# Kernel optimization log

Hardware: AMD Instinct MI355X
Metric: run time of the kernel (lower is better)

## Reference

```python
import jax, jax.numpy as jnp
import numpy as np

WS = (8, 8)
NUM_HEADS = 6
DIM = 192
HEAD_DIM = DIM // NUM_HEADS
SCALE = HEAD_DIM ** -0.5


def _relative_position_index(ws):
    ch, cw = np.arange(ws[0]), np.arange(ws[1])
    coords = np.stack(np.meshgrid(ch, cw, indexing='ij'))          # (2, Wh, Ww)
    cf = coords.reshape(2, -1)                                      # (2, N)
    rel = cf[:, :, None] - cf[:, None, :]                           # (2, N, N)
    rel = rel.transpose(1, 2, 0).copy()                             # (N, N, 2)
    rel[:, :, 0] += ws[0] - 1
    rel[:, :, 1] += ws[1] - 1
    rel[:, :, 0] *= 2 * ws[1] - 1
    return rel.sum(-1)                                              # (N, N)

REL_IDX = jnp.asarray(_relative_position_index(WS))


def setup_inputs() -> dict:
    key = jax.random.key(0)
    ks = jax.random.split(key, 9)
    B_, N, C = 8192, WS[0] * WS[1], DIM
    x1 = jax.random.normal(ks[0], (B_, N, C), jnp.float32)
    x2 = jax.random.normal(ks[1], (B_, N, C), jnp.float32)
    mask = jnp.zeros((1024, N, N), jnp.float32)
    q_w = jax.random.normal(ks[2], (C, C), jnp.float32) * 0.02
    q_b = jnp.zeros((C,), jnp.float32)
    kv_w = jax.random.normal(ks[3], (2 * C, C), jnp.float32) * 0.02
    kv_b = jnp.zeros((2 * C,), jnp.float32)
    proj_w = jax.random.normal(ks[4], (C, C), jnp.float32) * 0.02
    proj_b = jnp.zeros((C,), jnp.float32)
    table = jax.random.normal(ks[5], ((2 * WS[0] - 1) * (2 * WS[1] - 1), NUM_HEADS), jnp.float32) * 0.02
    return dict(x1=x1, x2=x2, mask=mask, q_w=q_w, q_b=q_b, kv_w=kv_w,
                kv_b=kv_b, proj_w=proj_w, proj_b=proj_b, table=table)


def reference(x1, x2, mask, q_w, q_b, kv_w, kv_b, proj_w, proj_b, table):
    B_, N, C = x1.shape
    H, hd = NUM_HEADS, HEAD_DIM
    q = (x1 @ q_w.T + q_b).reshape(B_, N, H, hd).transpose(0, 2, 1, 3)   # (B_,H,N,hd)
    kv = (x2 @ kv_w.T + kv_b).reshape(B_, N, 2, H, hd).transpose(2, 0, 3, 1, 4)
    k, v = kv[0], kv[1]                                                   # (B_,H,N,hd)
    attn = jnp.einsum('bhnd,bhmd->bhnm', q * SCALE, k)                    # (B_,H,N,N)
    bias = table[REL_IDX.reshape(-1)].reshape(N, N, H).transpose(2, 0, 1)  # (H,N,N)
    attn = attn + bias[None]
    nW = mask.shape[0]
    attn = attn.reshape(B_ // nW, nW, H, N, N) + mask[None, :, None]
    attn = jax.nn.softmax(attn.reshape(B_, H, N, N), axis=-1)
    out = jnp.einsum('bhnm,bhmd->bhnd', attn, v).transpose(0, 2, 1, 3).reshape(B_, N, C)
    return out @ proj_w.T + proj_b
```

## Files before the change

### kernel.cpp

```cpp
#include <hip/hip_runtime.h>

typedef __bf16 bf16_t;
typedef __bf16 bf16x8 __attribute__((ext_vector_type(8)));
typedef __bf16 bf16x4 __attribute__((ext_vector_type(4)));
typedef __bf16 bf16x2 __attribute__((ext_vector_type(2)));
typedef float f32x4 __attribute__((ext_vector_type(4)));

#define SCALE 0.17677669529663687f

__device__ __forceinline__ f32x4 mfma16(bf16x8 a, bf16x8 b, f32x4 c) {
  return __builtin_amdgcn_mfma_f32_16x16x32_bf16(a, b, c, 0, 0, 0);
}

__device__ __forceinline__ int swz(int row, int colByte, int strideB) {
  return row * strideB + ((((colByte >> 4) ^ (row & 7)) << 4) | (colByte & 15));
}

__device__ __forceinline__ void barrier_nd() {
  asm volatile("s_waitcnt lgkmcnt(0)" ::: "memory");
  __builtin_amdgcn_s_barrier();
  asm volatile("" ::: "memory");
}

union CvtU { bf16x2 h; unsigned int u; };
union PaU { unsigned int u[4]; bf16x8 v; };

__global__ void prep(const float* __restrict__ qw, const float* __restrict__ kvw,
                     const float* __restrict__ pw, bf16_t* __restrict__ wsb) {
  int i = blockIdx.x * 256 + threadIdx.x;
#pragma unroll
  for (int j = 0; j < 4; ++j) {
    int e = i * 4 + j;
    float v;
    if (e < 36864) v = qw[e] * SCALE;
    else if (e < 110592) v = kvw[e - 36864];
    else v = pw[e - 110592];
    wsb[e] = (bf16_t)v;
  }
}

template <bool WS>
__device__ __forceinline__ bf16x8 ldw(const bf16_t* __restrict__ wb,
                                      const float* __restrict__ wf, int off) {
  if constexpr (WS) {
    return *(const bf16x8*)(wb + off);
  } else {
    const float4* p = (const float4*)(wf + off);
    float4 a = p[0], c = p[1];
    bf16x8 r;
    r[0] = (bf16_t)a.x; r[1] = (bf16_t)a.y; r[2] = (bf16_t)a.z; r[3] = (bf16_t)a.w;
    r[4] = (bf16_t)c.x; r[5] = (bf16_t)c.y; r[6] = (bf16_t)c.z; r[7] = (bf16_t)c.w;
    return r;
  }
}

template <bool WS>
__global__ __launch_bounds__(512, 2) void wca_main(
    const float* __restrict__ x1, const float* __restrict__ x2,
    const float* __restrict__ mask,
    const float* __restrict__ qw_f, const float* __restrict__ qb,
    const float* __restrict__ kvw_f, const float* __restrict__ kvb,
    const float* __restrict__ pw_f, const float* __restrict__ pb,
    const float* __restrict__ table,
    const bf16_t* __restrict__ wsb,
    float* __restrict__ out) {
  extern __shared__ char smem[];
  char* RA = smem;
  char* RK = smem + 49152;
  char* RV = smem + 98304;

  const int t = threadIdx.x;
  const int w = t >> 6, l = t & 63, lo = l & 15, hi = l >> 4;
  const int win0 = 2 * blockIdx.x;

  const bf16_t* q_wb = wsb;
  const bf16_t* kv_wb = wsb + 36864;
  const bf16_t* p_wb = wsb + 110592;

  {
    const float4* s2a = (const float4*)(x2 + (size_t)win0 * 12288);
    const float4* s2b = (const float4*)(x2 + (size_t)(win0 + 1) * 12288);
    float4 ld[12];
#pragma unroll
    for (int it = 0; it < 3; ++it) {
      int idx = it * 512 + t;
      ld[4 * it + 0] = s2a[2 * idx]; ld[4 * it + 1] = s2a[2 * idx + 1];
      ld[4 * it + 2] = s2b[2 * idx]; ld[4 * it + 3] = s2b[2 * idx + 1];
    }
#pragma unroll
    for (int it = 0; it < 3; ++it) {
      int idx = it * 512 + t;
      int n = idx / 24, g = idx - n * 24;
      bf16x8 v;
      float4 a = ld[4 * it + 0], c = ld[4 * it + 1];
      v[0] = (bf16_t)a.x; v[1] = (bf16_t)a.y; v[2] = (bf16_t)a.z; v[3] = (bf16_t)a.w;
      v[4] = (bf16_t)c.x; v[5] = (bf16_t)c.y; v[6] = (bf16_t)c.z; v[7] = (bf16_t)c.w;
      *(bf16x8*)(RA + swz(n, g * 16, 384)) = v;
      a = ld[4 * it + 2]; c = ld[4 * it + 3];
      v[0] = (bf16_t)a.x; v[1] = (bf16_t)a.y; v[2] = (bf16_t)a.z; v[3] = (bf16_t)a.w;
      v[4] = (bf16_t)c.x; v[5] = (bf16_t)c.y; v[6] = (bf16_t)c.z; v[7] = (bf16_t)c.w;
      *(bf16x8*)(RA + swz(64 + n, g * 16, 384)) = v;
    }
  }
  barrier_nd();

  {
    bf16x8 wA[6][3];
#pragma unroll
    for (int kk = 0; kk < 6; ++kk)
#pragma unroll
      for (int ct = 0; ct < 3; ++ct) {
        int row = w * 48 + ct * 16 + lo;
        wA[kk][ct] = ldw<WS>(kv_wb, kvw_f, row * 192 + kk * 32 + hi * 8);
      }
    for (int wv = 0; wv < 2; ++wv) {
      f32x4 acc[4][3];
#pragma unroll
      for (int rt = 0; rt < 4; ++rt)
#pragma unroll
        for (int ct = 0; ct < 3; ++ct) { f32x4 z = {0.f, 0.f, 0.f, 0.f}; acc[rt][ct] = z; }
#pragma unroll
      for (int kk = 0; kk < 6; ++kk) {
        bf16x8 a[4];
#pragma unroll
        for (int rt = 0; rt < 4; ++rt)
          a[rt] = *(const bf16x8*)(RA + swz(wv * 64 + rt * 16 + lo, (kk * 4 + hi) * 16, 384));
#pragma unroll
        for (int rt = 0; rt < 4; ++rt)
#pragma unroll
          for (int ct = 0; ct < 3; ++ct)
            acc[rt][ct] = mfma16(a[rt], wA[kk][ct], acc[rt][ct]);
      }
      if (w < 4) {
#pragma unroll
        for (int ct = 0; ct < 3; ++ct) {
          int och = w * 48 + ct * 16 + lo;
          float bv = kvb[och];
#pragma unroll
          for (int rt = 0; rt < 4; ++rt)
#pragma unroll
            for (int i = 0; i < 4; ++i)
              *(bf16_t*)(RK + swz(wv * 64 + rt * 16 + hi * 4 + i, och * 2, 384)) =
                  (bf16_t)(acc[rt][ct][i] + bv);
        }
      } else {
#pragma unroll
        for (int ct = 0; ct < 3; ++ct) {
          int och = (w - 4) * 48 + ct * 16 + lo;
          float bv = kvb[192 + och];
#pragma unroll
          for (int rt = 0; rt < 4; ++rt) {
            int n0 = rt * 16 + hi * 4;
            bf16x4 pk;
#pragma unroll
            for (int i = 0; i < 4; ++i) pk[i] = (bf16_t)(acc[rt][ct][i] + bv);
            *(bf16x4*)(RV + wv * 24576 + swz(och, n0 * 2, 128)) = pk;
          }
        }
      }
    }
  }
  barrier_nd();

  {
    const int wv = w >> 2, rt2 = (w >> 1) & 1, cg = w & 1;
    const float* x1w = x1 + (size_t)(win0 + wv) * 12288;
    f32x4 acc[2][6];
#pragma unroll
    for (int rt = 0; rt < 2; ++rt)
#pragma unroll
      for (int ct = 0; ct < 6; ++ct) { f32x4 z = {0.f, 0.f, 0.f, 0.f}; acc[rt][ct] = z; }
#pragma unroll
    for (int kh = 0; kh < 2; ++kh) {
      float4 xf[2][3][2];
#pragma unroll
      for (int rt = 0; rt < 2; ++rt) {
        const float4* p = (const float4*)(x1w + (rt2 * 32 + rt * 16 + lo) * 192);
#pragma unroll
        for (int k2 = 0; k2 < 3; ++k2) {
          xf[rt][k2][0] = p[(kh * 3 + k2) * 8 + hi * 2];
          xf[rt][k2][1] = p[(kh * 3 + k2) * 8 + hi * 2 + 1];
        }
      }
      bf16x8 wB[3][6];
#pragma unroll
      for (int k2 = 0; k2 < 3; ++k2)
#pragma unroll
        for (int ct = 0; ct < 6; ++ct) {
          int col = cg * 96 + ct * 16 + lo;
          wB[k2][ct] = ldw<WS>(q_wb, qw_f, col * 192 + (kh * 3 + k2) * 32 + hi * 8);
        }
#pragma unroll
      for (int k2 = 0; k2 < 3; ++k2)
#pragma unroll
        for (int rt = 0; rt < 2; ++rt) {
          bf16x8 a;
          float4 xa = xf[rt][k2][0], xb = xf[rt][k2][1];
          a[0] = (bf16_t)xa.x; a[1] = (bf16_t)xa.y; a[2] = (bf16_t)xa.z; a[3] = (bf16_t)xa.w;
          a[4] = (bf16_t)xb.x; a[5] = (bf16_t)xb.y; a[6] = (bf16_t)xb.z; a[7] = (bf16_t)xb.w;
#pragma unroll
          for (int ct = 0; ct < 6; ++ct) acc[rt][ct] = mfma16(a, wB[k2][ct], acc[rt][ct]);
        }
    }
#pragma unroll
    for (int ct = 0; ct < 6; ++ct) {
      int col = cg * 96 + ct * 16 + lo;
      float qbs = qb[col] * SCALE;
#pragma unroll
      for (int rt = 0; rt < 2; ++rt)
#pragma unroll
        for (int i = 0; i < 4; ++i) {
          int row = wv * 64 + rt2 * 32 + rt * 16 + hi * 4 + i;
          float val = WS ? (acc[rt][ct][i] + qbs) : (acc[rt][ct][i] + qb[col]) * SCALE;
          *(bf16_t*)(RA + swz(row, col * 2, 384)) = (bf16_t)val;
        }
    }
  }
  barrier_nd();

  {
    const int wv = w >> 2, rt32 = (w >> 1) & 1, hh = w & 1;
    const int win = win0 + wv;
    const float* maskb = mask + (size_t)(win & 1023) * 4096;
    f32x4 mk[2][4];
    int ridx[2][4][4];
#pragma unroll
    for (int rts = 0; rts < 2; ++rts) {
      int r = rt32 * 32 + rts * 16 + lo;
#pragma unroll
      for (int ct = 0; ct < 4; ++ct) {
        mk[rts][ct] = *(const f32x4*)(maskb + r * 64 + ct * 16 + hi * 4);
#pragma unroll
        for (int i = 0; i < 4; ++i) {
          int c = ct * 16 + hi * 4 + i;
          ridx[rts][ct][i] = (((r >> 3) - (c >> 3) + 7) * 15 + ((r & 7) - (c & 7) + 7)) * 6;
        }
      }
    }
#pragma unroll
    for (int hq = 0; hq < 3; ++hq) {
      const int h = hh * 3 + hq;
#pragma unroll
      for (int rts = 0; rts < 2; ++rts) {
        const int rbase = rt32 * 32 + rts * 16;
        const int r = rbase + lo;
        bf16x8 qa = *(const bf16x8*)(RA + swz(wv * 64 + r, h * 64 + hi * 16, 384));
        f32x4 s[4];
#pragma unroll
        for (int ct = 0; ct < 4; ++ct) {
          f32x4 ci;
#pragma unroll
          for (int i = 0; i < 4; ++i) ci[i] = table[ridx[rts][ct][i] + h];
          ci += mk[rts][ct];
          bf16x8 ka = *(const bf16x8*)(RK + swz(wv * 64 + ct * 16 + lo, h * 64 + hi * 16, 384));
          s[ct] = mfma16(ka, qa, ci);
        }
        float mx = -1e30f;
#pragma unroll
        for (int ct = 0; ct < 4; ++ct)
#pragma unroll
          for (int i = 0; i < 4; ++i) mx = fmaxf(mx, s[ct][i]);
        mx = fmaxf(mx, __shfl_xor(mx, 16));
        mx = fmaxf(mx, __shfl_xor(mx, 32));
        float sum = 0.f;
#pragma unroll
        for (int ct = 0; ct < 4; ++ct)
#pragma unroll
          for (int i = 0; i < 4; ++i) {
            float p = __expf(s[ct][i] - mx);
            s[ct][i] = p;
            sum += p;
          }
        sum += __shfl_xor(sum, 16);
        sum += __shfl_xor(sum, 32);
        float rinv = 1.0f / sum;
        unsigned int word[4][2];
#pragma unroll
        for (int ct = 0; ct < 4; ++ct)
#pragma unroll
          for (int i2 = 0; i2 < 2; ++i2) {
            CvtU cu;
            cu.h[0] = (bf16_t)(s[ct][2 * i2] * rinv);
            cu.h[1] = (bf16_t)(s[ct][2 * i2 + 1] * rinv);
            word[ct][i2] = cu.u;
          }
        f32x4 o0 = {0.f, 0.f, 0.f, 0.f}, o1 = {0.f, 0.f, 0.f, 0.f};
#pragma unroll
        for (int k2 = 0; k2 < 2; ++k2) {
          PaU pa;
#pragma unroll
          for (int j2 = 0; j2 < 4; ++j2) {
            int src = lo + ((hi & 1) << 5) + ((j2 >> 1) << 4);
            unsigned int wa = (unsigned int)__shfl((int)word[2 * k2][j2 & 1], src);
            unsigned int wb = (unsigned int)__shfl((int)word[2 * k2 + 1][j2 & 1], src);
            pa.u[j2] = (hi & 2) ? wb : wa;
          }
          bf16x8 v0 = *(const bf16x8*)(RV + wv * 24576 + swz(h * 32 + lo, k2 * 64 + hi * 16, 128));
          bf16x8 v1 = *(const bf16x8*)(RV + wv * 24576 + swz(h * 32 + 16 + lo, k2 * 64 + hi * 16, 128));
          o0 = mfma16(pa.v, v0, o0);
          o1 = mfma16(pa.v, v1, o1);
        }
#pragma unroll
        for (int i = 0; i < 4; ++i) {
          int rr = wv * 64 + rbase + hi * 4 + i;
          *(bf16_t*)(RA + swz(rr, h * 64 + lo * 2, 384)) = (bf16_t)o0[i];
          *(bf16_t*)(RA + swz(rr, h * 64 + 32 + lo * 2, 384)) = (bf16_t)o1[i];
        }
      }
    }
  }
  barrier_nd();

  {
    const int wv = w >> 2, cgo = w & 3;
    bf16x8 wO[6][3];
#pragma unroll
    for (int kk = 0; kk < 6; ++kk)
#pragma unroll
      for (int ct = 0; ct < 3; ++ct) {
        int col = cgo * 48 + ct * 16 + lo;
        wO[kk][ct] = ldw<WS>(p_wb, pw_f, col * 192 + kk * 32 + hi * 8);
      }
    f32x4 acc[4][3];
#pragma unroll
    for (int rt = 0; rt < 4; ++rt)
#pragma unroll
      for (int ct = 0; ct < 3; ++ct) { f32x4 z = {0.f, 0.f, 0.f, 0.f}; acc[rt][ct] = z; }
#pragma unroll
    for (int kk = 0; kk < 6; ++kk) {
      bf16x8 a[4];
#pragma unroll
      for (int rt = 0; rt < 4; ++rt)
        a[rt] = *(const bf16x8*)(RA + swz(wv * 64 + rt * 16 + lo, (kk * 4 + hi) * 16, 384));
#pragma unroll
      for (int rt = 0; rt < 4; ++rt)
#pragma unroll
        for (int ct = 0; ct < 3; ++ct)
          acc[rt][ct] = mfma16(a[rt], wO[kk][ct], acc[rt][ct]);
    }
    float* outp = out + (size_t)(win0 + wv) * 12288;
#pragma unroll
    for (int ct = 0; ct < 3; ++ct) {
      int col = cgo * 48 + ct * 16 + lo;
      float bv = pb[col];
#pragma unroll
      for (int rt = 0; rt < 4; ++rt)
#pragma unroll
        for (int i = 0; i < 4; ++i)
          outp[(rt * 16 + hi * 4 + i) * 192 + col] = acc[rt][ct][i] + bv;
    }
  }
}

extern "C" void kernel_launch(void* const* d_in, const int* in_sizes, int n_in,
                              void* d_out, int out_size, void* d_ws, size_t ws_size,
                              hipStream_t stream) {
  const float* x1 = (const float*)d_in[0];
  const float* x2 = (const float*)d_in[1];
  const float* mask = (const float*)d_in[2];
  const float* qw = (const float*)d_in[3];
  const float* qb = (const float*)d_in[4];
  const float* kvw = (const float*)d_in[5];
  const float* kvb = (const float*)d_in[6];
  const float* pw = (const float*)d_in[7];
  const float* pb = (const float*)d_in[8];
  const float* table = (const float*)d_in[9];
  float* out = (float*)d_out;
  bf16_t* wsb = (bf16_t*)d_ws;
  const int LDS_BYTES = 147456;
  if (ws_size >= 294912) {
    prep<<<144, 256, 0, stream>>>(qw, kvw, pw, wsb);
    wca_main<true><<<4096, 512, LDS_BYTES, stream>>>(x1, x2, mask, qw, qb, kvw, kvb,
                                                     pw, pb, table, wsb, out);
  } else {
    wca_main<false><<<4096, 512, LDS_BYTES, stream>>>(x1, x2, mask, qw, qb, kvw, kvb,
                                                      pw, pb, table, wsb, out);
  }
}
```

Baseline: 651.9 us.

## Make kernel persistent over windows with async global-to-LDS prefetch of inputs

Replaces the one-block-per-two-windows launch (4096 blocks) with 256 persistent blocks that each loop over 32 windows, one window per iteration. The x2 and x1 fp32 tiles are fetched into an LDS staging buffer with global_load_lds DMA, so the next window's loads overlap the current window's compute. This is meant to hide global memory latency and cut per-block launch and setup overhead. In exchange each block handles a single window at a time, LDS use drops, there are more barriers per window, and 256 blocks may under-fill the GPU's compute units and leave occupancy low.

```diff
diff --git a/kernel.cpp b/kernel.cpp
--- a/kernel.cpp
+++ b/kernel.cpp
@@ -1,4 +1,5 @@
 #include <hip/hip_runtime.h>
+#include <stdint.h>
 
 typedef __bf16 bf16_t;
 typedef __bf16 bf16x8 __attribute__((ext_vector_type(8)));
@@ -20,6 +21,18 @@
   asm volatile("s_waitcnt lgkmcnt(0)" ::: "memory");
   __builtin_amdgcn_s_barrier();
   asm volatile("" ::: "memory");
+}
+__device__ __forceinline__ void barrier_vm() {
+  asm volatile("s_waitcnt vmcnt(0) lgkmcnt(0)" ::: "memory");
+  __builtin_amdgcn_s_barrier();
+  asm volatile("" ::: "memory");
+}
+
+__device__ __forceinline__ void dma16(const float* g, char* lds) {
+  __builtin_amdgcn_global_load_lds(
+      (const __attribute__((address_space(1))) uint32_t*)(uintptr_t)g,
+      (__attribute__((address_space(3))) uint32_t*)(uint32_t)(uintptr_t)lds,
+      16, 0, 0);
 }
 
 union CvtU { bf16x2 h; unsigned int u; };
@@ -66,54 +79,64 @@
     float* __restrict__ out) {
   extern __shared__ char smem[];
   char* RA = smem;
-  char* RK = smem + 49152;
-  char* RV = smem + 98304;
+  char* RK = smem + 24576;
+  char* RV = smem + 49152;
+  char* PF = smem + 73728;
 
   const int t = threadIdx.x;
   const int w = t >> 6, l = t & 63, lo = l & 15, hi = l >> 4;
-  const int win0 = 2 * blockIdx.x;
+  const int bid = blockIdx.x;
+  const int rtB = w & 3, cgB = w >> 2;
 
   const bf16_t* q_wb = wsb;
   const bf16_t* kv_wb = wsb + 36864;
   const bf16_t* p_wb = wsb + 110592;
 
   {
-    const float4* s2a = (const float4*)(x2 + (size_t)win0 * 12288);
-    const float4* s2b = (const float4*)(x2 + (size_t)(win0 + 1) * 12288);
-    float4 ld[12];
-#pragma unroll
-    for (int it = 0; it < 3; ++it) {
-      int idx = it * 512 + t;
-      ld[4 * it + 0] = s2a[2 * idx]; ld[4 * it + 1] = s2a[2 * idx + 1];
-      ld[4 * it + 2] = s2b[2 * idx]; ld[4 * it + 3] = s2b[2 * idx + 1];
-    }
-#pragma unroll
-    for (int it = 0; it < 3; ++it) {
-      int idx = it * 512 + t;
-      int n = idx / 24, g = idx - n * 24;
-      bf16x8 v;
-      float4 a = ld[4 * it + 0], c = ld[4 * it + 1];
-      v[0] = (bf16_t)a.x; v[1] = (bf16_t)a.y; v[2] = (bf16_t)a.z; v[3] = (bf16_t)a.w;
-      v[4] = (bf16_t)c.x; v[5] = (bf16_t)c.y; v[6] = (bf16_t)c.z; v[7] = (bf16_t)c.w;
-      *(bf16x8*)(RA + swz(n, g * 16, 384)) = v;
-      a = ld[4 * it + 2]; c = ld[4 * it + 3];
-      v[0] = (bf16_t)a.x; v[1] = (bf16_t)a.y; v[2] = (bf16_t)a.z; v[3] = (bf16_t)a.w;
-      v[4] = (bf16_t)c.x; v[5] = (bf16_t)c.y; v[6] = (bf16_t)c.z; v[7] = (bf16_t)c.w;
-      *(bf16x8*)(RA + swz(64 + n, g * 16, 384)) = v;
-    }
-  }
-  barrier_nd();
-
-  {
-    bf16x8 wA[6][3];
-#pragma unroll
-    for (int kk = 0; kk < 6; ++kk)
-#pragma unroll
-      for (int ct = 0; ct < 3; ++ct) {
-        int row = w * 48 + ct * 16 + lo;
-        wA[kk][ct] = ldw<WS>(kv_wb, kvw_f, row * 192 + kk * 32 + hi * 8);
-      }
-    for (int wv = 0; wv < 2; ++wv) {
+    const float* x2w = x2 + (size_t)bid * 12288;
+#pragma unroll
+    for (int k = 0; k < 6; ++k)
+      dma16(x2w + ((w * 6 + k) * 64 + l) * 4, PF + (w * 6 + k) * 1024);
+  }
+
+#pragma unroll 1
+  for (int j = 0; j < 32; ++j) {
+    const int win = j * 256 + bid;
+
+    barrier_vm();
+
+#pragma unroll
+    for (int it = 0; it < 6; ++it) {
+      int G = it * 512 + t;
+      f32x4 v = *(const f32x4*)(PF + G * 16);
+      bf16x4 o;
+      o[0] = (bf16_t)v[0]; o[1] = (bf16_t)v[1];
+      o[2] = (bf16_t)v[2]; o[3] = (bf16_t)v[3];
+      int n = G / 48, cb = (G - n * 48) * 8;
+      *(bf16x4*)(RA + swz(n, cb, 384)) = o;
+    }
+    barrier_nd();
+
+    {
+      const float* x1w = x1 + (size_t)win * 12288;
+#pragma unroll
+      for (int k = 0; k < 6; ++k) {
+        int P = (w * 6 + k) * 64 + l;
+        int row = P / 48, c = P - row * 48;
+        int Lg = row * 48 + (c ^ (row & 7));
+        dma16(x1w + Lg * 4, PF + P * 16);
+      }
+    }
+
+    {
+      bf16x8 wA[6][3];
+#pragma unroll
+      for (int kk = 0; kk < 6; ++kk)
+#pragma unroll
+        for (int ct = 0; ct < 3; ++ct) {
+          int row = w * 48 + ct * 16 + lo;
+          wA[kk][ct] = ldw<WS>(kv_wb, kvw_f, row * 192 + kk * 32 + hi * 8);
+        }
       f32x4 acc[4][3];
 #pragma unroll
       for (int rt = 0; rt < 4; ++rt)
@@ -124,7 +147,7 @@
         bf16x8 a[4];
 #pragma unroll
         for (int rt = 0; rt < 4; ++rt)
-          a[rt] = *(const bf16x8*)(RA + swz(wv * 64 + rt * 16 + lo, (kk * 4 + hi) * 16, 384));
+          a[rt] = *(const bf16x8*)(RA + swz(rt * 16 + lo, (kk * 4 + hi) * 16, 384));
 #pragma unroll
         for (int rt = 0; rt < 4; ++rt)
 #pragma unroll
@@ -140,7 +163,7 @@
           for (int rt = 0; rt < 4; ++rt)
 #pragma unroll
             for (int i = 0; i < 4; ++i)
-              *(bf16_t*)(RK + swz(wv * 64 + rt * 16 + hi * 4 + i, och * 2, 384)) =
+              *(bf16_t*)(RK + swz(rt * 16 + hi * 4 + i, och * 2, 384)) =
                   (bf16_t)(acc[rt][ct][i] + bv);
         }
       } else {
@@ -154,106 +177,96 @@
             bf16x4 pk;
 #pragma unroll
             for (int i = 0; i < 4; ++i) pk[i] = (bf16_t)(acc[rt][ct][i] + bv);
-            *(bf16x4*)(RV + wv * 24576 + swz(och, n0 * 2, 128)) = pk;
-          }
-        }
-      }
-    }
-  }
-  barrier_nd();
-
-  {
-    const int wv = w >> 2, rt2 = (w >> 1) & 1, cg = w & 1;
-    const float* x1w = x1 + (size_t)(win0 + wv) * 12288;
-    f32x4 acc[2][6];
-#pragma unroll
-    for (int rt = 0; rt < 2; ++rt)
-#pragma unroll
-      for (int ct = 0; ct < 6; ++ct) { f32x4 z = {0.f, 0.f, 0.f, 0.f}; acc[rt][ct] = z; }
-#pragma unroll
-    for (int kh = 0; kh < 2; ++kh) {
-      float4 xf[2][3][2];
-#pragma unroll
-      for (int rt = 0; rt < 2; ++rt) {
-        const float4* p = (const float4*)(x1w + (rt2 * 32 + rt * 16 + lo) * 192);
+            *(bf16x4*)(RV + swz(och, n0 * 2, 128)) = pk;
+          }
+        }
+      }
+    }
+    barrier_vm();
+
+    {
+      const int arow = rtB * 16 + lo;
+      const int xr = arow & 7;
+      const char* PFrow = PF + arow * 768;
+      f32x4 acc[6];
+#pragma unroll
+      for (int ct = 0; ct < 6; ++ct) { f32x4 z = {0.f, 0.f, 0.f, 0.f}; acc[ct] = z; }
+#pragma unroll
+      for (int kh = 0; kh < 2; ++kh) {
+        bf16x8 wB[3][6];
+#pragma unroll
+        for (int k2 = 0; k2 < 3; ++k2)
+#pragma unroll
+          for (int ct = 0; ct < 6; ++ct) {
+            int col = cgB * 96 + ct * 16 + lo;
+            wB[k2][ct] = ldw<WS>(q_wb, qw_f, col * 192 + (kh * 3 + k2) * 32 + hi * 8);
+          }
 #pragma unroll
         for (int k2 = 0; k2 < 3; ++k2) {
-          xf[rt][k2][0] = p[(kh * 3 + k2) * 8 + hi * 2];
-          xf[rt][k2][1] = p[(kh * 3 + k2) * 8 + hi * 2 + 1];
-        }
-      }
-      bf16x8 wB[3][6];
-#pragma unroll
-      for (int k2 = 0; k2 < 3; ++k2)
-#pragma unroll
-        for (int ct = 0; ct < 6; ++ct) {
-          int col = cg * 96 + ct * 16 + lo;
-          wB[k2][ct] = ldw<WS>(q_wb, qw_f, col * 192 + (kh * 3 + k2) * 32 + hi * 8);
-        }
-#pragma unroll
-      for (int k2 = 0; k2 < 3; ++k2)
-#pragma unroll
-        for (int rt = 0; rt < 2; ++rt) {
+          int c0 = (kh * 3 + k2) * 8 + hi * 2;
+          int p0 = c0 ^ xr;
+          f32x4 va = *(const f32x4*)(PFrow + p0 * 16);
+          f32x4 vb = *(const f32x4*)(PFrow + (p0 ^ 1) * 16);
           bf16x8 a;
-          float4 xa = xf[rt][k2][0], xb = xf[rt][k2][1];
-          a[0] = (bf16_t)xa.x; a[1] = (bf16_t)xa.y; a[2] = (bf16_t)xa.z; a[3] = (bf16_t)xa.w;
-          a[4] = (bf16_t)xb.x; a[5] = (bf16_t)xb.y; a[6] = (bf16_t)xb.z; a[7] = (bf16_t)xb.w;
-#pragma unroll
-          for (int ct = 0; ct < 6; ++ct) acc[rt][ct] = mfma16(a, wB[k2][ct], acc[rt][ct]);
-        }
-    }
-#pragma unroll
-    for (int ct = 0; ct < 6; ++ct) {
-      int col = cg * 96 + ct * 16 + lo;
-      float qbs = qb[col] * SCALE;
-#pragma unroll
-      for (int rt = 0; rt < 2; ++rt)
+          a[0] = (bf16_t)va[0]; a[1] = (bf16_t)va[1];
+          a[2] = (bf16_t)va[2]; a[3] = (bf16_t)va[3];
+          a[4] = (bf16_t)vb[0]; a[5] = (bf16_t)vb[1];
+          a[6] = (bf16_t)vb[2]; a[7] = (bf16_t)vb[3];
+#pragma unroll
+          for (int ct = 0; ct < 6; ++ct) acc[ct] = mfma16(a, wB[k2][ct], acc[ct]);
+        }
+      }
+#pragma unroll
+      for (int ct = 0; ct < 6; ++ct) {
+        int col = cgB * 96 + ct * 16 + lo;
 #pragma unroll
         for (int i = 0; i < 4; ++i) {
-          int row = wv * 64 + rt2 * 32 + rt * 16 + hi * 4 + i;
-          float val = WS ? (acc[rt][ct][i] + qbs) : (acc[rt][ct][i] + qb[col]) * SCALE;
-          *(bf16_t*)(RA + swz(row, col * 2, 384)) = (bf16_t)val;
-        }
-    }
-  }
-  barrier_nd();
-
-  {
-    const int wv = w >> 2, rt32 = (w >> 1) & 1, hh = w & 1;
-    const int win = win0 + wv;
-    const float* maskb = mask + (size_t)(win & 1023) * 4096;
-    f32x4 mk[2][4];
-    int ridx[2][4][4];
-#pragma unroll
-    for (int rts = 0; rts < 2; ++rts) {
-      int r = rt32 * 32 + rts * 16 + lo;
+          float val = WS ? (acc[ct][i] + qb[col] * SCALE)
+                         : (acc[ct][i] + qb[col]) * SCALE;
+          *(bf16_t*)(RA + swz(rtB * 16 + hi * 4 + i, col * 2, 384)) = (bf16_t)val;
+        }
+      }
+    }
+    barrier_nd();
+
+    if (j < 31) {
+      const float* x2w = x2 + (size_t)(win + 256) * 12288;
+#pragma unroll
+      for (int k = 0; k < 6; ++k)
+        dma16(x2w + ((w * 6 + k) * 64 + l) * 4, PF + (w * 6 + k) * 1024);
+    }
+
+    {
+      const int rt3 = w >> 1, hh = w & 1, rbase = rt3 * 16;
+      const int r = rbase + lo;
+      const float* maskp = mask + (size_t)(win & 1023) * 4096 + r * 64;
+      f32x4 mk[4];
+      int ridx[4][4];
 #pragma unroll
       for (int ct = 0; ct < 4; ++ct) {
-        mk[rts][ct] = *(const f32x4*)(maskb + r * 64 + ct * 16 + hi * 4);
+        mk[ct] = *(const f32x4*)(maskp + ct * 16 + hi * 4);
 #pragma unroll
         for (int i = 0; i < 4; ++i) {
           int c = ct * 16 + hi * 4 + i;
-          ridx[rts][ct][i] = (((r >> 3) - (c >> 3) + 7) * 15 + ((r & 7) - (c & 7) + 7)) * 6;
-        }
-      }
-    }
-#pragma unroll
-    for (int hq = 0; hq < 3; ++hq) {
-      const int h = hh * 3 + hq;
-#pragma unroll
-      for (int rts = 0; rts < 2; ++rts) {
-        const int rbase = rt32 * 32 + rts * 16;
-        const int r = rbase + lo;
-        bf16x8 qa = *(const bf16x8*)(RA + swz(wv * 64 + r, h * 64 + hi * 16, 384));
+          ridx[ct][i] = (((r >> 3) - (c >> 3) + 7) * 15 + ((r & 7) - (c & 7) + 7)) * 6;
+        }
+      }
+#pragma unroll
+      for (int hq = 0; hq < 3; ++hq) {
+        const int h = hh * 3 + hq;
+        f32x4 cb[4];
+#pragma unroll
+        for (int ct = 0; ct < 4; ++ct) {
+#pragma unroll
+          for (int i = 0; i < 4; ++i) cb[ct][i] = table[ridx[ct][i] + h];
+          cb[ct] += mk[ct];
+        }
+        bf16x8 qa = *(const bf16x8*)(RA + swz(r, h * 64 + hi * 16, 384));
         f32x4 s[4];
 #pragma unroll
         for (int ct = 0; ct < 4; ++ct) {
-          f32x4 ci;
-#pragma unroll
-          for (int i = 0; i < 4; ++i) ci[i] = table[ridx[rts][ct][i] + h];
-          ci += mk[rts][ct];
-          bf16x8 ka = *(const bf16x8*)(RK + swz(wv * 64 + ct * 16 + lo, h * 64 + hi * 16, 384));
-          s[ct] = mfma16(ka, qa, ci);
+          bf16x8 ka = *(const bf16x8*)(RK + swz(ct * 16 + lo, h * 64 + hi * 16, 384));
+          s[ct] = mfma16(ka, qa, cb[ct]);
         }
         float mx = -1e30f;
 #pragma unroll
@@ -295,59 +308,52 @@
             unsigned int wb = (unsigned int)__shfl((int)word[2 * k2 + 1][j2 & 1], src);
             pa.u[j2] = (hi & 2) ? wb : wa;
           }
-          bf16x8 v0 = *(const bf16x8*)(RV + wv * 24576 + swz(h * 32 + lo, k2 * 64 + hi * 16, 128));
-          bf16x8 v1 = *(const bf16x8*)(RV + wv * 24576 + swz(h * 32 + 16 + lo, k2 * 64 + hi * 16, 128));
+          bf16x8 v0 = *(const bf16x8*)(RV + swz(h * 32 + lo, k2 * 64 + hi * 16, 128));
+          bf16x8 v1 = *(const bf16x8*)(RV + swz(h * 32 + 16 + lo, k2 * 64 + hi * 16, 128));
           o0 = mfma16(pa.v, v0, o0);
           o1 = mfma16(pa.v, v1, o1);
         }
 #pragma unroll
         for (int i = 0; i < 4; ++i) {
-          int rr = wv * 64 + rbase + hi * 4 + i;
+          int rr = rbase + hi * 4 + i;
           *(bf16_t*)(RA + swz(rr, h * 64 + lo * 2, 384)) = (bf16_t)o0[i];
           *(bf16_t*)(RA + swz(rr, h * 64 + 32 + lo * 2, 384)) = (bf16_t)o1[i];
         }
       }
     }
-  }
-  barrier_nd();
-
-  {
-    const int wv = w >> 2, cgo = w & 3;
-    bf16x8 wO[6][3];
-#pragma unroll
-    for (int kk = 0; kk < 6; ++kk)
-#pragma unroll
-      for (int ct = 0; ct < 3; ++ct) {
-        int col = cgo * 48 + ct * 16 + lo;
-        wO[kk][ct] = ldw<WS>(p_wb, pw_f, col * 192 + kk * 32 + hi * 8);
-      }
-    f32x4 acc[4][3];
-#pragma unroll
-    for (int rt = 0; rt < 4; ++rt)
-#pragma unroll
-      for (int ct = 0; ct < 3; ++ct) { f32x4 z = {0.f, 0.f, 0.f, 0.f}; acc[rt][ct] = z; }
-#pragma unroll
-    for (int kk = 0; kk < 6; ++kk) {
-      bf16x8 a[4];
-#pragma unroll
-      for (int rt = 0; rt < 4; ++rt)
-        a[rt] = *(const bf16x8*)(RA + swz(wv * 64 + rt * 16 + lo, (kk * 4 + hi) * 16, 384));
-#pragma unroll
-      for (int rt = 0; rt < 4; ++rt)
-#pragma unroll
-        for (int ct = 0; ct < 3; ++ct)
-          acc[rt][ct] = mfma16(a[rt], wO[kk][ct], acc[rt][ct]);
-    }
-    float* outp = out + (size_t)(win0 + wv) * 12288;
-#pragma unroll
-    for (int ct = 0; ct < 3; ++ct) {
-      int col = cgo * 48 + ct * 16 + lo;
-      float bv = pb[col];
-#pragma unroll
-      for (int rt = 0; rt < 4; ++rt)
+    barrier_nd();
+
+    {
+      f32x4 acc[6];
+#pragma unroll
+      for (int ct = 0; ct < 6; ++ct) { f32x4 z = {0.f, 0.f, 0.f, 0.f}; acc[ct] = z; }
+#pragma unroll
+      for (int kh = 0; kh < 2; ++kh) {
+        bf16x8 wB[3][6];
+#pragma unroll
+        for (int k2 = 0; k2 < 3; ++k2)
+#pragma unroll
+          for (int ct = 0; ct < 6; ++ct) {
+            int col = cgB * 96 + ct * 16 + lo;
+            wB[k2][ct] = ldw<WS>(p_wb, pw_f, col * 192 + (kh * 3 + k2) * 32 + hi * 8);
+          }
+#pragma unroll
+        for (int k2 = 0; k2 < 3; ++k2) {
+          bf16x8 a = *(const bf16x8*)(
+              RA + swz(rtB * 16 + lo, ((kh * 3 + k2) * 4 + hi) * 16, 384));
+#pragma unroll
+          for (int ct = 0; ct < 6; ++ct) acc[ct] = mfma16(a, wB[k2][ct], acc[ct]);
+        }
+      }
+      float* outp = out + (size_t)win * 12288;
+#pragma unroll
+      for (int ct = 0; ct < 6; ++ct) {
+        int col = cgB * 96 + ct * 16 + lo;
+        float bv = pb[col];
 #pragma unroll
         for (int i = 0; i < 4; ++i)
-          outp[(rt * 16 + hi * 4 + i) * 192 + col] = acc[rt][ct][i] + bv;
+          outp[(rtB * 16 + hi * 4 + i) * 192 + col] = acc[ct][i] + bv;
+      }
     }
   }
 }
@@ -367,13 +373,13 @@
   const float* table = (const float*)d_in[9];
   float* out = (float*)d_out;
   bf16_t* wsb = (bf16_t*)d_ws;
-  const int LDS_BYTES = 147456;
+  const int LDS_BYTES = 122880;
   if (ws_size >= 294912) {
     prep<<<144, 256, 0, stream>>>(qw, kvw, pw, wsb);
-    wca_main<true><<<4096, 512, LDS_BYTES, stream>>>(x1, x2, mask, qw, qb, kvw, kvb,
+    wca_main<true><<<256, 512, LDS_BYTES, stream>>>(x1, x2, mask, qw, qb, kvw, kvb,
+                                                    pw, pb, table, wsb, out);
+  } else {
+    wca_main<false><<<256, 512, LDS_BYTES, stream>>>(x1, x2, mask, qw, qb, kvw, kvb,
                                                      pw, pb, table, wsb, out);
-  } else {
-    wca_main<false><<<4096, 512, LDS_BYTES, stream>>>(x1, x2, mask, qw, qb, kvw, kvb,
-                                                      pw, pb, table, wsb, out);
-  }
-}
+  }
+}
```

After: 1.789 ms. +174.4%, slower.

## Double block to 1024 threads and redistribute work across sixteen waves

Applied to the files above, without the earlier changes.

Launches 1024 threads per block instead of 512 and re-partitions every stage (x2 staging, KV projection, Q projection, attention, output projection) so each wave handles a smaller slice. Weight fragments are now loaded per k-step inside the loop rather than preloaded, which lowers register pressure. The aim is more waves in flight per CU to hide latency. LDS use stays at 144KB per block, so only one block fits per CU, and the __launch_bounds__(1024,4) hint cannot actually be met.

```diff
diff --git a/kernel.cpp b/kernel.cpp
--- a/kernel.cpp
+++ b/kernel.cpp
@@ -55,7 +55,7 @@
 }
 
 template <bool WS>
-__global__ __launch_bounds__(512, 2) void wca_main(
+__global__ __launch_bounds__(1024, 4) void wca_main(
     const float* __restrict__ x1, const float* __restrict__ x2,
     const float* __restrict__ mask,
     const float* __restrict__ qw_f, const float* __restrict__ qb,
@@ -71,6 +71,7 @@
 
   const int t = threadIdx.x;
   const int w = t >> 6, l = t & 63, lo = l & 15, hi = l >> 4;
+  const int wv = w >> 3, u = w & 7;
   const int win0 = 2 * blockIdx.x;
 
   const bf16_t* q_wb = wsb;
@@ -80,263 +81,224 @@
   {
     const float4* s2a = (const float4*)(x2 + (size_t)win0 * 12288);
     const float4* s2b = (const float4*)(x2 + (size_t)(win0 + 1) * 12288);
-    float4 ld[12];
 #pragma unroll
     for (int it = 0; it < 3; ++it) {
-      int idx = it * 512 + t;
-      ld[4 * it + 0] = s2a[2 * idx]; ld[4 * it + 1] = s2a[2 * idx + 1];
-      ld[4 * it + 2] = s2b[2 * idx]; ld[4 * it + 3] = s2b[2 * idx + 1];
-    }
-#pragma unroll
-    for (int it = 0; it < 3; ++it) {
-      int idx = it * 512 + t;
-      int n = idx / 24, g = idx - n * 24;
-      bf16x8 v;
-      float4 a = ld[4 * it + 0], c = ld[4 * it + 1];
-      v[0] = (bf16_t)a.x; v[1] = (bf16_t)a.y; v[2] = (bf16_t)a.z; v[3] = (bf16_t)a.w;
-      v[4] = (bf16_t)c.x; v[5] = (bf16_t)c.y; v[6] = (bf16_t)c.z; v[7] = (bf16_t)c.w;
-      *(bf16x8*)(RA + swz(n, g * 16, 384)) = v;
-      a = ld[4 * it + 2]; c = ld[4 * it + 3];
-      v[0] = (bf16_t)a.x; v[1] = (bf16_t)a.y; v[2] = (bf16_t)a.z; v[3] = (bf16_t)a.w;
-      v[4] = (bf16_t)c.x; v[5] = (bf16_t)c.y; v[6] = (bf16_t)c.z; v[7] = (bf16_t)c.w;
-      *(bf16x8*)(RA + swz(64 + n, g * 16, 384)) = v;
+      int G = it * 1024 + t;
+      int n = G / 48, g = G - n * 48;
+      float4 a = s2a[G];
+      bf16x4 o;
+      o[0] = (bf16_t)a.x; o[1] = (bf16_t)a.y; o[2] = (bf16_t)a.z; o[3] = (bf16_t)a.w;
+      *(bf16x4*)(RA + swz(n, g * 8, 384)) = o;
+      a = s2b[G];
+      o[0] = (bf16_t)a.x; o[1] = (bf16_t)a.y; o[2] = (bf16_t)a.z; o[3] = (bf16_t)a.w;
+      *(bf16x4*)(RA + swz(64 + n, g * 8, 384)) = o;
     }
   }
   barrier_nd();
 
   {
-    bf16x8 wA[6][3];
-#pragma unroll
-    for (int kk = 0; kk < 6; ++kk)
+    const int part = u >> 2;
+    const int kcol = (u & 3) * 48;
+    f32x4 acc[4][3];
+#pragma unroll
+    for (int rt = 0; rt < 4; ++rt)
+#pragma unroll
+      for (int ct = 0; ct < 3; ++ct) { f32x4 z = {0.f, 0.f, 0.f, 0.f}; acc[rt][ct] = z; }
+#pragma unroll
+    for (int kk = 0; kk < 6; ++kk) {
+      bf16x8 a[4];
+#pragma unroll
+      for (int rt = 0; rt < 4; ++rt)
+        a[rt] = *(const bf16x8*)(RA + swz(wv * 64 + rt * 16 + lo, (kk * 4 + hi) * 16, 384));
+      bf16x8 bw[3];
 #pragma unroll
       for (int ct = 0; ct < 3; ++ct) {
-        int row = w * 48 + ct * 16 + lo;
-        wA[kk][ct] = ldw<WS>(kv_wb, kvw_f, row * 192 + kk * 32 + hi * 8);
-      }
-    for (int wv = 0; wv < 2; ++wv) {
-      f32x4 acc[4][3];
+        int row = part * 192 + kcol + ct * 16 + lo;
+        bw[ct] = ldw<WS>(kv_wb, kvw_f, row * 192 + kk * 32 + hi * 8);
+      }
 #pragma unroll
       for (int rt = 0; rt < 4; ++rt)
 #pragma unroll
-        for (int ct = 0; ct < 3; ++ct) { f32x4 z = {0.f, 0.f, 0.f, 0.f}; acc[rt][ct] = z; }
-#pragma unroll
-      for (int kk = 0; kk < 6; ++kk) {
-        bf16x8 a[4];
+        for (int ct = 0; ct < 3; ++ct)
+          acc[rt][ct] = mfma16(a[rt], bw[ct], acc[rt][ct]);
+    }
+    if (part == 0) {
+#pragma unroll
+      for (int ct = 0; ct < 3; ++ct) {
+        int och = kcol + ct * 16 + lo;
+        float bv = kvb[och];
 #pragma unroll
         for (int rt = 0; rt < 4; ++rt)
-          a[rt] = *(const bf16x8*)(RA + swz(wv * 64 + rt * 16 + lo, (kk * 4 + hi) * 16, 384));
-#pragma unroll
-        for (int rt = 0; rt < 4; ++rt)
-#pragma unroll
-          for (int ct = 0; ct < 3; ++ct)
-            acc[rt][ct] = mfma16(a[rt], wA[kk][ct], acc[rt][ct]);
-      }
-      if (w < 4) {
-#pragma unroll
-        for (int ct = 0; ct < 3; ++ct) {
-          int och = w * 48 + ct * 16 + lo;
-          float bv = kvb[och];
-#pragma unroll
-          for (int rt = 0; rt < 4; ++rt)
-#pragma unroll
-            for (int i = 0; i < 4; ++i)
-              *(bf16_t*)(RK + swz(wv * 64 + rt * 16 + hi * 4 + i, och * 2, 384)) =
-                  (bf16_t)(acc[rt][ct][i] + bv);
+#pragma unroll
+          for (int i = 0; i < 4; ++i)
+            *(bf16_t*)(RK + swz(wv * 64 + rt * 16 + hi * 4 + i, och * 2, 384)) =
+                (bf16_t)(acc[rt][ct][i] + bv);
+      }
+    } else {
+#pragma unroll
+      for (int ct = 0; ct < 3; ++ct) {
+        int och = kcol + ct * 16 + lo;
+        float bv = kvb[192 + och];
+#pragma unroll
+        for (int rt = 0; rt < 4; ++rt) {
+          int n0 = rt * 16 + hi * 4;
+          bf16x4 pk;
+#pragma unroll
+          for (int i = 0; i < 4; ++i) pk[i] = (bf16_t)(acc[rt][ct][i] + bv);
+          *(bf16x4*)(RV + wv * 24576 + swz(och, n0 * 2, 128)) = pk;
         }
-      } else {
-#pragma unroll
-        for (int ct = 0; ct < 3; ++ct) {
-          int och = (w - 4) * 48 + ct * 16 + lo;
-          float bv = kvb[192 + och];
-#pragma unroll
-          for (int rt = 0; rt < 4; ++rt) {
-            int n0 = rt * 16 + hi * 4;
-            bf16x4 pk;
-#pragma unroll
-            for (int i = 0; i < 4; ++i) pk[i] = (bf16_t)(acc[rt][ct][i] + bv);
-            *(bf16x4*)(RV + wv * 24576 + swz(och, n0 * 2, 128)) = pk;
-          }
-        }
       }
     }
   }
   barrier_nd();
 
   {
-    const int wv = w >> 2, rt2 = (w >> 1) & 1, cg = w & 1;
-    const float* x1w = x1 + (size_t)(win0 + wv) * 12288;
-    f32x4 acc[2][6];
-#pragma unroll
-    for (int rt = 0; rt < 2; ++rt)
-#pragma unroll
-      for (int ct = 0; ct < 6; ++ct) { f32x4 z = {0.f, 0.f, 0.f, 0.f}; acc[rt][ct] = z; }
-#pragma unroll
-    for (int kh = 0; kh < 2; ++kh) {
-      float4 xf[2][3][2];
-#pragma unroll
-      for (int rt = 0; rt < 2; ++rt) {
-        const float4* p = (const float4*)(x1w + (rt2 * 32 + rt * 16 + lo) * 192);
-#pragma unroll
-        for (int k2 = 0; k2 < 3; ++k2) {
-          xf[rt][k2][0] = p[(kh * 3 + k2) * 8 + hi * 2];
-          xf[rt][k2][1] = p[(kh * 3 + k2) * 8 + hi * 2 + 1];
-        }
-      }
-      bf16x8 wB[3][6];
-#pragma unroll
-      for (int k2 = 0; k2 < 3; ++k2)
-#pragma unroll
-        for (int ct = 0; ct < 6; ++ct) {
-          int col = cg * 96 + ct * 16 + lo;
-          wB[k2][ct] = ldw<WS>(q_wb, qw_f, col * 192 + (kh * 3 + k2) * 32 + hi * 8);
-        }
-#pragma unroll
-      for (int k2 = 0; k2 < 3; ++k2)
-#pragma unroll
-        for (int rt = 0; rt < 2; ++rt) {
-          bf16x8 a;
-          float4 xa = xf[rt][k2][0], xb = xf[rt][k2][1];
-          a[0] = (bf16_t)xa.x; a[1] = (bf16_t)xa.y; a[2] = (bf16_t)xa.z; a[3] = (bf16_t)xa.w;
-          a[4] = (bf16_t)xb.x; a[5] = (bf16_t)xb.y; a[6] = (bf16_t)xb.z; a[7] = (bf16_t)xb.w;
-#pragma unroll
-          for (int ct = 0; ct < 6; ++ct) acc[rt][ct] = mfma16(a, wB[k2][ct], acc[rt][ct]);
-        }
+    const int rt = u & 3, cg = u >> 2;
+    const float4* p = (const float4*)(x1 + (size_t)(win0 + wv) * 12288 + (rt * 16 + lo) * 192);
+    f32x4 acc[6];
+#pragma unroll
+    for (int ct = 0; ct < 6; ++ct) { f32x4 z = {0.f, 0.f, 0.f, 0.f}; acc[ct] = z; }
+#pragma unroll
+    for (int kk = 0; kk < 6; ++kk) {
+      float4 xa = p[kk * 8 + hi * 2], xb = p[kk * 8 + hi * 2 + 1];
+      bf16x8 wB[6];
+#pragma unroll
+      for (int ct = 0; ct < 6; ++ct) {
+        int col = cg * 96 + ct * 16 + lo;
+        wB[ct] = ldw<WS>(q_wb, qw_f, col * 192 + kk * 32 + hi * 8);
+      }
+      bf16x8 a;
+      a[0] = (bf16_t)xa.x; a[1] = (bf16_t)xa.y; a[2] = (bf16_t)xa.z; a[3] = (bf16_t)xa.w;
+      a[4] = (bf16_t)xb.x; a[5] = (bf16_t)xb.y; a[6] = (bf16_t)xb.z; a[7] = (bf16_t)xb.w;
+#pragma unroll
+      for (int ct = 0; ct < 6; ++ct) acc[ct] = mfma16(a, wB[ct], acc[ct]);
     }
 #pragma unroll
     for (int ct = 0; ct < 6; ++ct) {
       int col = cg * 96 + ct * 16 + lo;
-      float qbs = qb[col] * SCALE;
-#pragma unroll
-      for (int rt = 0; rt < 2; ++rt)
-#pragma unroll
-        for (int i = 0; i < 4; ++i) {
-          int row = wv * 64 + rt2 * 32 + rt * 16 + hi * 4 + i;
-          float val = WS ? (acc[rt][ct][i] + qbs) : (acc[rt][ct][i] + qb[col]) * SCALE;
-          *(bf16_t*)(RA + swz(row, col * 2, 384)) = (bf16_t)val;
-        }
+#pragma unroll
+      for (int i = 0; i < 4; ++i) {
+        float val = WS ? (acc[ct][i] + qb[col] * SCALE)
+                       : (acc[ct][i] + qb[col]) * SCALE;
+        *(bf16_t*)(RA + swz(wv * 64 + rt * 16 + hi * 4 + i, col * 2, 384)) = (bf16_t)val;
+      }
     }
   }
   barrier_nd();
 
   {
-    const int wv = w >> 2, rt32 = (w >> 1) & 1, hh = w & 1;
+    const int rt16 = u >> 1, hh = u & 1, rbase = rt16 * 16;
+    const int r = rbase + lo;
     const int win = win0 + wv;
-    const float* maskb = mask + (size_t)(win & 1023) * 4096;
-    f32x4 mk[2][4];
-    int ridx[2][4][4];
-#pragma unroll
-    for (int rts = 0; rts < 2; ++rts) {
-      int r = rt32 * 32 + rts * 16 + lo;
-#pragma unroll
-      for (int ct = 0; ct < 4; ++ct) {
-        mk[rts][ct] = *(const f32x4*)(maskb + r * 64 + ct * 16 + hi * 4);
-#pragma unroll
-        for (int i = 0; i < 4; ++i) {
-          int c = ct * 16 + hi * 4 + i;
-          ridx[rts][ct][i] = (((r >> 3) - (c >> 3) + 7) * 15 + ((r & 7) - (c & 7) + 7)) * 6;
-        }
+    const float* maskp = mask + (size_t)(win & 1023) * 4096 + r * 64;
+    f32x4 mk[4];
+    int ridx[4][4];
+#pragma unroll
+    for (int ct = 0; ct < 4; ++ct) {
+      mk[ct] = *(const f32x4*)(maskp + ct * 16 + hi * 4);
+#pragma unroll
+      for (int i = 0; i < 4; ++i) {
+        int c = ct * 16 + hi * 4 + i;
+        ridx[ct][i] = (((r >> 3) - (c >> 3) + 7) * 15 + ((r & 7) - (c & 7) + 7)) * 6;
       }
     }
 #pragma unroll
     for (int hq = 0; hq < 3; ++hq) {
       const int h = hh * 3 + hq;
-#pragma unroll
-      for (int rts = 0; rts < 2; ++rts) {
-        const int rbase = rt32 * 32 + rts * 16;
-        const int r = rbase + lo;
-        bf16x8 qa = *(const bf16x8*)(RA + swz(wv * 64 + r, h * 64 + hi * 16, 384));
-        f32x4 s[4];
-#pragma unroll
-        for (int ct = 0; ct < 4; ++ct) {
-          f32x4 ci;
-#pragma unroll
-          for (int i = 0; i < 4; ++i) ci[i] = table[ridx[rts][ct][i] + h];
-          ci += mk[rts][ct];
-          bf16x8 ka = *(const bf16x8*)(RK + swz(wv * 64 + ct * 16 + lo, h * 64 + hi * 16, 384));
-          s[ct] = mfma16(ka, qa, ci);
+      f32x4 cb[4];
+#pragma unroll
+      for (int ct = 0; ct < 4; ++ct) {
+#pragma unroll
+        for (int i = 0; i < 4; ++i) cb[ct][i] = table[ridx[ct][i] + h];
+        cb[ct] += mk[ct];
+      }
+      bf16x8 qa = *(const bf16x8*)(RA + swz(wv * 64 + r, h * 64 + hi * 16, 384));
+      f32x4 s[4];
+#pragma unroll
+      for (int ct = 0; ct < 4; ++ct) {
+        bf16x8 ka = *(const bf16x8*)(RK + swz(wv * 64 + ct * 16 + lo, h * 64 + hi * 16, 384));
+        s[ct] = mfma16(ka, qa, cb[ct]);
+      }
+      float mx = -1e30f;
+#pragma unroll
+      for (int ct = 0; ct < 4; ++ct)
+#pragma unroll
+        for (int i = 0; i < 4; ++i) mx = fmaxf(mx, s[ct][i]);
+      mx = fmaxf(mx, __shfl_xor(mx, 16));
+      mx = fmaxf(mx, __shfl_xor(mx, 32));
+      float sum = 0.f;
+#pragma unroll
+      for (int ct = 0; ct < 4; ++ct)
+#pragma unroll
+        for (int i = 0; i < 4; ++i) {
+          float p = __expf(s[ct][i] - mx);
+          s[ct][i] = p;
+          sum += p;
         }
-        float mx = -1e30f;
-#pragma unroll
-        for (int ct = 0; ct < 4; ++ct)
-#pragma unroll
-          for (int i = 0; i < 4; ++i) mx = fmaxf(mx, s[ct][i]);
-        mx = fmaxf(mx, __shfl_xor(mx, 16));
-        mx = fmaxf(mx, __shfl_xor(mx, 32));
-        float sum = 0.f;
-#pragma unroll
-        for (int ct = 0; ct < 4; ++ct)
-#pragma unroll
-          for (int i = 0; i < 4; ++i) {
-            float p = __expf(s[ct][i] - mx);
-            s[ct][i] = p;
-            sum += p;
-          }
-        sum += __shfl_xor(sum, 16);
-        sum += __shfl_xor(sum, 32);
-        float rinv = 1.0f / sum;
-        unsigned int word[4][2];
-#pragma unroll
-        for (int ct = 0; ct < 4; ++ct)
-#pragma unroll
-          for (int i2 = 0; i2 < 2; ++i2) {
-            CvtU cu;
-            cu.h[0] = (bf16_t)(s[ct][2 * i2] * rinv);
-            cu.h[1] = (bf16_t)(s[ct][2 * i2 + 1] * rinv);
-            word[ct][i2] = cu.u;
-          }
-        f32x4 o0 = {0.f, 0.f, 0.f, 0.f}, o1 = {0.f, 0.f, 0.f, 0.f};
-#pragma unroll
-        for (int k2 = 0; k2 < 2; ++k2) {
-          PaU pa;
-#pragma unroll
-          for (int j2 = 0; j2 < 4; ++j2) {
-            int src = lo + ((hi & 1) << 5) + ((j2 >> 1) << 4);
-            unsigned int wa = (unsigned int)__shfl((int)word[2 * k2][j2 & 1], src);
-            unsigned int wb = (unsigned int)__shfl((int)word[2 * k2 + 1][j2 & 1], src);
-            pa.u[j2] = (hi & 2) ? wb : wa;
-          }
-          bf16x8 v0 = *(const bf16x8*)(RV + wv * 24576 + swz(h * 32 + lo, k2 * 64 + hi * 16, 128));
-          bf16x8 v1 = *(const bf16x8*)(RV + wv * 24576 + swz(h * 32 + 16 + lo, k2 * 64 + hi * 16, 128));
-          o0 = mfma16(pa.v, v0, o0);
-          o1 = mfma16(pa.v, v1, o1);
+      sum += __shfl_xor(sum, 16);
+      sum += __shfl_xor(sum, 32);
+      float rinv = 1.0f / sum;
+      unsigned int word[4][2];
+#pragma unroll
+      for (int ct = 0; ct < 4; ++ct)
+#pragma unroll
+        for (int i2 = 0; i2 < 2; ++i2) {
+          CvtU cu;
+          cu.h[0] = (bf16_t)(s[ct][2 * i2] * rinv);
+          cu.h[1] = (bf16_t)(s[ct][2 * i2 + 1] * rinv);
+          word[ct][i2] = cu.u;
         }
-#pragma unroll
-        for (int i = 0; i < 4; ++i) {
-          int rr = wv * 64 + rbase + hi * 4 + i;
-          *(bf16_t*)(RA + swz(rr, h * 64 + lo * 2, 384)) = (bf16_t)o0[i];
-          *(bf16_t*)(RA + swz(rr, h * 64 + 32 + lo * 2, 384)) = (bf16_t)o1[i];
+      f32x4 o0 = {0.f, 0.f, 0.f, 0.f}, o1 = {0.f, 0.f, 0.f, 0.f};
+#pragma unroll
+      for (int k2 = 0; k2 < 2; ++k2) {
+        PaU pa;
+#pragma unroll
+        for (int j2 = 0; j2 < 4; ++j2) {
+          int src = lo + ((hi & 1) << 5) + ((j2 >> 1) << 4);
+          unsigned int wa = (unsigned int)__shfl((int)word[2 * k2][j2 & 1], src);
+          unsigned int wb = (unsigned int)__shfl((int)word[2 * k2 + 1][j2 & 1], src);
+          pa.u[j2] = (hi & 2) ? wb : wa;
         }
+        bf16x8 v0 = *(const bf16x8*)(RV + wv * 24576 + swz(h * 32 + lo, k2 * 64 + hi * 16, 128));
+        bf16x8 v1 = *(const bf16x8*)(RV + wv * 24576 + swz(h * 32 + 16 + lo, k2 * 64 + hi * 16, 128));
+        o0 = mfma16(pa.v, v0, o0);
+        o1 = mfma16(pa.v, v1, o1);
+      }
+#pragma unroll
+      for (int i = 0; i < 4; ++i) {
+        int rr = wv * 64 + rbase + hi * 4 + i;
+        *(bf16_t*)(RA + swz(rr, h * 64 + lo * 2, 384)) = (bf16_t)o0[i];
+        *(bf16_t*)(RA + swz(rr, h * 64 + 32 + lo * 2, 384)) = (bf16_t)o1[i];
       }
     }
   }
   barrier_nd();
 
   {
-    const int wv = w >> 2, cgo = w & 3;
-    bf16x8 wO[6][3];
-#pragma unroll
-    for (int kk = 0; kk < 6; ++kk)
+    const int ro = u >> 2, cgo = u & 3;
+    f32x4 acc[2][3];
+#pragma unroll
+    for (int rt = 0; rt < 2; ++rt)
+#pragma unroll
+      for (int ct = 0; ct < 3; ++ct) { f32x4 z = {0.f, 0.f, 0.f, 0.f}; acc[rt][ct] = z; }
+#pragma unroll
+    for (int kk = 0; kk < 6; ++kk) {
+      bf16x8 a[2];
+#pragma unroll
+      for (int rt = 0; rt < 2; ++rt)
+        a[rt] = *(const bf16x8*)(
+            RA + swz(wv * 64 + ro * 32 + rt * 16 + lo, (kk * 4 + hi) * 16, 384));
+      bf16x8 wO[3];
 #pragma unroll
       for (int ct = 0; ct < 3; ++ct) {
         int col = cgo * 48 + ct * 16 + lo;
-        wO[kk][ct] = ldw<WS>(p_wb, pw_f, col * 192 + kk * 32 + hi * 8);
-      }
-    f32x4 acc[4][3];
-#pragma unroll
-    for (int rt = 0; rt < 4; ++rt)
-#pragma unroll
-      for (int ct = 0; ct < 3; ++ct) { f32x4 z = {0.f, 0.f, 0.f, 0.f}; acc[rt][ct] = z; }
-#pragma unroll
-    for (int kk = 0; kk < 6; ++kk) {
-      bf16x8 a[4];
-#pragma unroll
-      for (int rt = 0; rt < 4; ++rt)
-        a[rt] = *(const bf16x8*)(RA + swz(wv * 64 + rt * 16 + lo, (kk * 4 + hi) * 16, 384));
-#pragma unroll
-      for (int rt = 0; rt < 4; ++rt)
+        wO[ct] = ldw<WS>(p_wb, pw_f, col * 192 + kk * 32 + hi * 8);
+      }
+#pragma unroll
+      for (int rt = 0; rt < 2; ++rt)
 #pragma unroll
         for (int ct = 0; ct < 3; ++ct)
-          acc[rt][ct] = mfma16(a[rt], wO[kk][ct], acc[rt][ct]);
+          acc[rt][ct] = mfma16(a[rt], wO[ct], acc[rt][ct]);
     }
     float* outp = out + (size_t)(win0 + wv) * 12288;
 #pragma unroll
@@ -344,10 +306,10 @@
       int col = cgo * 48 + ct * 16 + lo;
       float bv = pb[col];
 #pragma unroll
-      for (int rt = 0; rt < 4; ++rt)
+      for (int rt = 0; rt < 2; ++rt)
 #pragma unroll
         for (int i = 0; i < 4; ++i)
-          outp[(rt * 16 + hi * 4 + i) * 192 + col] = acc[rt][ct][i] + bv;
+          outp[(ro * 32 + rt * 16 + hi * 4 + i) * 192 + col] = acc[rt][ct][i] + bv;
     }
   }
 }
@@ -370,10 +332,10 @@
   const int LDS_BYTES = 147456;
   if (ws_size >= 294912) {
     prep<<<144, 256, 0, stream>>>(qw, kvw, pw, wsb);
-    wca_main<true><<<4096, 512, LDS_BYTES, stream>>>(x1, x2, mask, qw, qb, kvw, kvb,
-                                                     pw, pb, table, wsb, out);
+    wca_main<true><<<4096, 1024, LDS_BYTES, stream>>>(x1, x2, mask, qw, qb, kvw, kvb,
+                                                      pw, pb, table, wsb, out);
   } else {
-    wca_main<false><<<4096, 512, LDS_BYTES, stream>>>(x1, x2, mask, qw, qb, kvw, kvb,
-                                                      pw, pb, table, wsb, out);
-  }
-}
+    wca_main<false><<<4096, 1024, LDS_BYTES, stream>>>(x1, x2, mask, qw, qb, kvw, kvb,
+                                                       pw, pb, table, wsb, out);
+  }
+}
```

Result: slower. 853.8 us (+31.0%).
